# Kernel tuning notes

Measured on AMD Instinct MI355X. Metric: run time of the kernel, lower is better.

## Reference

```python
import jax, jax.numpy as jnp
import numpy as np

T, IN, OUT, M, C = 8192, 1024, 1024, 128, 32
MIN_PERIOD, MAX_PERIOD = 1.0, 1024.0
LN_EPS = 1e-5


def _linear_params(key, in_f, out_f):
    # equinox nn.Linear default init: U(-1/sqrt(in), 1/sqrt(in)) for weight and bias
    lim = 1.0 / np.sqrt(in_f)
    kw, kb = jax.random.split(key)
    w = jax.random.uniform(kw, (out_f, in_f), minval=-lim, maxval=lim, dtype=jnp.float32)
    b = jax.random.uniform(kb, (out_f,), minval=-lim, maxval=lim, dtype=jnp.float32)
    return w, b


def setup_inputs() -> dict:
    key = jax.random.key(0)
    ks = jax.random.split(key, 8)
    x = jax.random.normal(ks[0], (T, IN), dtype=jnp.float32)
    done = jax.random.bernoulli(ks[1], 0.01, (T,))  # sparse episode resets
    state_re = jnp.zeros((1, M, C), jnp.float32)
    state_im = jnp.zeros((1, M, C), jnp.float32)
    # ffa.init(memory_size, context_size): decay rates a and context frequencies b
    a = jnp.linspace(1e-6, 0.5, M, dtype=jnp.float32)
    b = 2.0 * jnp.pi / jnp.linspace(MIN_PERIOD, MAX_PERIOD, C, dtype=jnp.float32)
    pre_w, pre_b = _linear_params(ks[2], IN, M)
    gin_w, gin_b = _linear_params(ks[3], IN, M)
    gout_w, gout_b = _linear_params(ks[4], IN, OUT)
    skip_w, skip_b = _linear_params(ks[5], IN, OUT)
    mix_w, mix_b = _linear_params(ks[6], 2 * M * C, OUT)
    return dict(x=x, done=done, state_re=state_re, state_im=state_im, a=a, b=b,
                pre_w=pre_w, pre_b=pre_b, gin_w=gin_w, gin_b=gin_b,
                gout_w=gout_w, gout_b=gout_b, skip_w=skip_w, skip_b=skip_b,
                mix_w=mix_w, mix_b=mix_b)


def _ffm_forward(x, done, s0, a, b, pre_w, pre_b, gin_w, gin_b,
                 gout_w, gout_b, skip_w, skip_b, mix_w, mix_b):
    # input gating: gated_x[t, m]
    gate_in = jax.nn.sigmoid(x @ gin_w.T + gin_b)            # [T, M]
    gated_x = (x @ pre_w.T + pre_b) * gate_in                # [T, M]

    # gamma[m, c] = exp(-|a_m| + i b_c): per-step complex decay/rotation
    re, im = jnp.broadcast_arrays(-jnp.abs(a)[:, None], b[None, :])
    gamma = jnp.exp(jax.lax.complex(re, im))                 # [M, C] complex64

    def step(s, inp):
        # s_t = gamma * s_{t-1} * (1 - done_t) + x_t 1^T  (reset before accumulate)
        xt, dt = inp
        keep = jnp.where(dt, 0.0, 1.0).astype(jnp.float32)
        s = keep * s * gamma + xt[:, None]
        return s, s

    _, states = jax.lax.scan(step, s0, (gated_x.astype(jnp.complex64), done))  # [T, M, C]

    # mix: concat(real, imag) along last axis -> [T, M, 2C] -> [T, 2MC]
    z_in = jnp.concatenate([states.real, states.imag], axis=-1).reshape(states.shape[0], -1)
    z = z_in @ mix_w.T + mix_b                               # [T, OUT]

    gate_out = jax.nn.sigmoid(x @ gout_w.T + gout_b)         # [T, OUT]
    skip = x @ skip_w.T + skip_b                             # [T, OUT]

    # LayerNorm without weight/bias (eps = 1e-5)
    zg = z * gate_out
    mu = zg.mean(-1, keepdims=True)
    var = ((zg - mu) ** 2).mean(-1, keepdims=True)
    ln = (zg - mu) / jnp.sqrt(var + LN_EPS)

    out = ln + skip * (1.0 - gate_out)
    return out, states


def reference(x, done, state_re, state_im, a, b, pre_w, pre_b, gin_w, gin_b,
              gout_w, gout_b, skip_w, skip_b, mix_w, mix_b):
    s0 = jax.lax.complex(state_re, state_im)[0]              # [M, C]
    return _ffm_forward(x, done, s0, a, b, pre_w, pre_b, gin_w, gin_b,
                        gout_w, gout_b, skip_w, skip_b, mix_w, mix_b)
```

## Files before the change

### kernel.cpp

```cpp
#include <hip/hip_runtime.h>
#include <stdint.h>

#define T_DIM 8192
#define IN_DIM 1024
#define OUT_DIM 1024
#define M_DIM 128
#define SEG 64
#define NSEG (T_DIM / SEG)
#define CHUNK 2048
#define KS_FB 4

typedef __bf16 bf16x8 __attribute__((ext_vector_type(8)));
typedef float f32x4 __attribute__((ext_vector_type(4)));

__device__ inline unsigned short f2bf(float f) {
  unsigned int u = __float_as_uint(f);
  unsigned int r = (u + 0x7fffu + ((u >> 16) & 1u)) >> 16;
  return (unsigned short)r;
}
__device__ inline float bf2f(unsigned short h) {
  return __uint_as_float(((unsigned int)h) << 16);
}
__device__ inline float sigm(float v) { return 1.f / (1.f + expf(-v)); }

#define N_X   8388608L
#define N_MIX 8388608L
#define N_WGS 2359296L
__global__ __launch_bounds__(256) void prep_kernel(
    const float* __restrict__ x, const float* __restrict__ mix_w,
    const float* __restrict__ gout_w, const float* __restrict__ skip_w,
    const float* __restrict__ pre_w, const float* __restrict__ gin_w,
    const float* __restrict__ gout_b, const float* __restrict__ skip_b,
    const float* __restrict__ pre_b, const float* __restrict__ gin_b,
    const float* __restrict__ a, const float* __restrict__ b,
    unsigned short* __restrict__ x_bf, unsigned short* __restrict__ Bmix,
    unsigned short* __restrict__ Wgs, float* __restrict__ bias_gs,
    float2* __restrict__ gam, float2* __restrict__ gamL) {
  const long total = N_X + N_MIX + N_WGS + 2304 + 4096;
  for (long i = (long)blockIdx.x * 256 + threadIdx.x; i < total;
       i += (long)gridDim.x * 256) {
    if (i < N_X) {
      x_bf[i] = f2bf(x[i]);
    } else if (i < N_X + N_MIX) {
      long j = i - N_X;
      long row = j >> 13;
      int k = (int)(j & 8191);
      int src = ((k >> 6) << 6) | ((k & 1) << 5) | ((k >> 1) & 31);
      Bmix[j] = f2bf(mix_w[(row << 13) + src]);
    } else if (i < N_X + N_MIX + N_WGS) {
      long j = i - N_X - N_MIX;
      int row = (int)(j >> 10), col = (int)(j & 1023);
      float v;
      if (row < 1024)       v = gout_w[row * 1024 + col];
      else if (row < 2048)  v = skip_w[(row - 1024) * 1024 + col];
      else if (row < 2176)  v = pre_w[(row - 2048) * 1024 + col];
      else                  v = gin_w[(row - 2176) * 1024 + col];
      Wgs[j] = f2bf(v);
    } else if (i < N_X + N_MIX + N_WGS + 2304) {
      int j = (int)(i - N_X - N_MIX - N_WGS);
      float v;
      if (j < 1024)      v = gout_b[j];
      else if (j < 2048) v = skip_b[j - 1024];
      else if (j < 2176) v = pre_b[j - 2048];
      else               v = gin_b[j - 2176];
      bias_gs[j] = v;
    } else {
      int tid = (int)(i - N_X - N_MIX - N_WGS - 2304);
      int m = tid >> 5, c = tid & 31;
      double aa = fabs((double)a[m]);
      double ang = (double)b[c];
      double mag = exp(-aa);
      gam[tid] = make_float2((float)(mag * cos(ang)), (float)(mag * sin(ang)));
      double magL = exp(-aa * (double)SEG);
      double angL = ang * (double)SEG;
      gamL[tid] = make_float2((float)(magL * cos(angL)), (float)(magL * sin(angL)));
    }
  }
}

#define GEMM_KLOOP(AP, BP, LDK)                                                        \
  for (int k0 = 0; k0 < kloop_end; k0 += 64) {                                         \
    _Pragma("unroll")                                                                  \
    for (int cc = 0; cc < 4; ++cc) {                                                   \
      __builtin_amdgcn_global_load_lds(                                                \
          (const __attribute__((address_space(1))) void*)(AP + k0 + (size_t)cc * 32 * (LDK)), \
          (__attribute__((address_space(3))) void*)(As + cc * 2048 + w * 512), 16, 0, 0);     \
      __builtin_amdgcn_global_load_lds(                                                \
          (const __attribute__((address_space(1))) void*)(BP + k0 + (size_t)cc * 32 * (LDK)), \
          (__attribute__((address_space(3))) void*)(Bs + cc * 2048 + w * 512), 16, 0, 0);     \
    }                                                                                  \
    __syncthreads();                                                                   \
    _Pragma("unroll")                                                                  \
    for (int kk = 0; kk < 2; ++kk) {                                                   \
      const int eb = kk ? e1 : e0;                                                     \
      const char* Bp = (const char*)Bpbase + eb;                                       \
      bf16x8 b0 = *(const bf16x8*)(Bp);                                                \
      bf16x8 b1 = *(const bf16x8*)(Bp + 2048);                                         \
      bf16x8 b2 = *(const bf16x8*)(Bp + 4096);                                         \
      bf16x8 b3 = *(const bf16x8*)(Bp + 6144);                                         \
      const char* Ap = (const char*)Apbase + eb;                                       \
      _Pragma("unroll")                                                                \
      for (int i = 0; i < 4; ++i) {                                                    \
        bf16x8 af = *(const bf16x8*)(Ap + i * 2048);                                   \
        acc[i][0] = __builtin_amdgcn_mfma_f32_16x16x32_bf16(af, b0, acc[i][0], 0, 0, 0);\
        acc[i][1] = __builtin_amdgcn_mfma_f32_16x16x32_bf16(af, b1, acc[i][1], 0, 0, 0);\
        acc[i][2] = __builtin_amdgcn_mfma_f32_16x16x32_bf16(af, b2, acc[i][2], 0, 0, 0);\
        acc[i][3] = __builtin_amdgcn_mfma_f32_16x16x32_bf16(af, b3, acc[i][3], 0, 0, 0);\
      }                                                                                \
    }                                                                                  \
    __syncthreads();                                                                   \
  }

#define GEMM_PREAMBLE                                                                  \
  const int tid = threadIdx.x;                                                         \
  const int lane = tid & 63, w = tid >> 6;                                             \
  const int wr = w >> 1, wc = w & 1;                                                   \
  f32x4 acc[4][4] = {};                                                                \
  const int srow = tid >> 3;                                                           \
  const int ksw = ((tid & 7) ^ (srow & 7)) * 8;                                        \
  const int l15 = lane & 15;                                                           \
  const int krd = (lane >> 4) * 8;                                                     \
  const int rsw = (lane & 7) << 3;                                                     \
  const int e0 = (krd ^ rsw) * 2;                                                      \
  const int e1 = ((32 + krd) ^ rsw) * 2;                                               \
  const unsigned short* Apbase = &As[(wr * 64 + l15) * 64];                            \
  const unsigned short* Bpbase = &Bs[(wc * 64 + l15) * 64];

__global__ __launch_bounds__(256, 4) void gemm_gs_kernel(
    const unsigned short* __restrict__ A, const unsigned short* __restrict__ B,
    const float* __restrict__ bias, unsigned short* __restrict__ gs,
    float* __restrict__ tmp) {
  __shared__ __align__(16) unsigned short As[128 * 64];
  __shared__ __align__(16) unsigned short Bs[128 * 64];
  const int xcd = blockIdx.x & 7;
  const int idx = blockIdx.x >> 3;
  const int bn = idx % 18;
  const int bm = xcd * 8 + idx / 18;
  const int n0 = bn * 128, t0 = bm * 128;
  GEMM_PREAMBLE
  const unsigned short* Ab = A + (size_t)(t0 + srow) * 1024 + ksw;
  const unsigned short* Bb = B + (size_t)(n0 + srow) * 1024 + ksw;
  const int kloop_end = 1024;
  GEMM_KLOOP(Ab, Bb, 1024)

  const int rbase = t0 + wr * 64 + ((lane >> 4) * 4);
  const int cbase = n0 + wc * 64 + l15;
#pragma unroll
  for (int j = 0; j < 4; ++j) {
    const int col = cbase + j * 16;
    const float bv = bias[col];
#pragma unroll
    for (int i = 0; i < 4; ++i) {
#pragma unroll
      for (int r = 0; r < 4; ++r) {
        float v = acc[i][j][r] + bv;
        int row = rbase + i * 16 + r;
        if (col < 2048) gs[(size_t)row * 2048 + col] = f2bf(v);
        else            tmp[(size_t)row * 256 + (col - 2048)] = v;
      }
    }
  }
}

__global__ __launch_bounds__(256, 4) void gemm_splitk_kernel(
    const unsigned short* __restrict__ A, const unsigned short* __restrict__ B,
    float* __restrict__ partials, int nbm, int kslice, int prows, int xcd_map) {
  __shared__ __align__(16) unsigned short As[128 * 64];
  __shared__ __align__(16) unsigned short Bs[128 * 64];
  int bm, bn, ks;
  if (xcd_map) {
    const int xcd = blockIdx.x & 7;
    const int idx = blockIdx.x >> 3;
    ks = xcd >> 2;
    bm = (xcd & 3) * 16 + (idx >> 3);
    bn = idx & 7;
  } else {
    const int cpx = gridDim.x >> 3;
    const int wid = (blockIdx.x & 7) * cpx + (blockIdx.x >> 3);
    bm = wid % nbm;
    bn = (wid / nbm) & 7;
    ks = wid / (nbm * 8);
  }
  const int n0 = bn * 128, t0 = bm * 128;
  GEMM_PREAMBLE
  const unsigned short* Ab = A + (size_t)(t0 + srow) * 8192 + ks * kslice + ksw;
  const unsigned short* Bb = B + (size_t)(n0 + srow) * 8192 + ks * kslice + ksw;
  const int kloop_end = kslice;
  GEMM_KLOOP(Ab, Bb, 8192)

  float* Cp = partials + (size_t)ks * prows * 1024;
  const int rbase = t0 + wr * 64 + ((lane >> 4) * 4);
  const int cbase = n0 + wc * 64 + l15;
#pragma unroll
  for (int j = 0; j < 4; ++j) {
    const int col = cbase + j * 16;
#pragma unroll
    for (int i = 0; i < 4; ++i)
#pragma unroll
      for (int r = 0; r < 4; ++r)
        Cp[(size_t)(rbase + i * 16 + r) * 1024 + col] = acc[i][j][r];
  }
}

__global__ __launch_bounds__(256) void reduce_kernel(const f32x4* __restrict__ partials,
                                                     const f32x4* __restrict__ bias4,
                                                     f32x4* __restrict__ outc) {
  int i = blockIdx.x * 256 + threadIdx.x;
  const size_t stride = (size_t)CHUNK * 256;
  f32x4 s = partials[i];
#pragma unroll
  for (int p = 1; p < KS_FB; ++p) s += partials[(size_t)p * stride + i];
  s += bias4[i & 255];
  outc[i] = s;
}

__global__ __launch_bounds__(256) void gated_kernel(const float* __restrict__ tmp,
                                                    float* __restrict__ gated) {
  int i = blockIdx.x * 256 + threadIdx.x;
  int t = i >> 7, m = i & 127;
  float p = tmp[t * 256 + m];
  float g = tmp[t * 256 + 128 + m];
  gated[i] = p * sigm(g);
}

__global__ __launch_bounds__(256) void scan_p1_kernel(
    const float* __restrict__ gated, const int* __restrict__ done,
    const float2* __restrict__ gam, const float2* __restrict__ gamL,
    float2* __restrict__ carryA, float2* __restrict__ carryB) {
  int gid = blockIdx.x * 256 + threadIdx.x;
  int seg = gid >> 12, tid = gid & 4095;
  int m = tid >> 5;
  float2 g = gam[tid];
  int t0 = seg * SEG;
  float sr = 0.f, si = 0.f, keep_all = 1.f;
  for (int tt = 0; tt < SEG; ++tt) {
    int t = t0 + tt;
    float xv = gated[t * M_DIM + m];
    bool d = done[t] != 0;
    float pr = d ? 0.f : sr;
    float pi = d ? 0.f : si;
    if (d) keep_all = 0.f;
    sr = fmaf(g.x, pr, fmaf(-g.y, pi, xv));
    si = fmaf(g.y, pr, g.x * pi);
  }
  carryB[(size_t)seg * 4096 + tid] = make_float2(sr, si);
  float2 gL = gamL[tid];
  carryA[(size_t)seg * 4096 + tid] = make_float2(keep_all * gL.x, keep_all * gL.y);
}

__global__ __launch_bounds__(256) void scan_p2_kernel(
    const float2* __restrict__ carryA, float2* __restrict__ carryB,
    const float* __restrict__ s0_re, const float* __restrict__ s0_im) {
  int tid = blockIdx.x * 256 + threadIdx.x;
  float sr = s0_re[tid], si = s0_im[tid];
  float2 A0 = carryA[tid], B0 = carryB[tid];
  for (int p = 0; p < NSEG; ++p) {
    size_t nidx = (size_t)(p + 1) * 4096 + tid;
    float2 A1, B1;
    if (p + 1 < NSEG) { A1 = carryA[nidx]; B1 = carryB[nidx]; }
    carryB[(size_t)p * 4096 + tid] = make_float2(sr, si);
    float nr = fmaf(A0.x, sr, fmaf(-A0.y, si, B0.x));
    float ni = fmaf(A0.y, sr, fmaf(A0.x, si, B0.y));
    sr = nr; si = ni;
    A0 = A1; B0 = B1;
  }
}

__global__ __launch_bounds__(256) void scan_p3_kernel(
    const float* __restrict__ gated, const int* __restrict__ done,
    const float2* __restrict__ gam, const float2* __restrict__ segstart,
    float* __restrict__ out_states, int pair_mode,
    unsigned int* __restrict__ st_bf, int tbase) {
  int gid = blockIdx.x * 256 + threadIdx.x;
  int segl = gid >> 12, tid = gid & 4095;
  int m = tid >> 5;
  int seg = tbase / SEG + segl;
  float2 g = gam[tid];
  float2 s = segstart[(size_t)seg * 4096 + tid];
  float sr = s.x, si = s.y;
  int t0 = seg * SEG;
  for (int tt = 0; tt < SEG; ++tt) {
    int t = t0 + tt;
    float xv = gated[t * M_DIM + m];
    bool d = done[t] != 0;
    float pr = d ? 0.f : sr;
    float pi = d ? 0.f : si;
    sr = fmaf(g.x, pr, fmaf(-g.y, pi, xv));
    si = fmaf(g.y, pr, g.x * pi);
    if (pair_mode) {
      ((float2*)out_states)[(size_t)t * 4096 + tid] = make_float2(sr, si);
    } else {
      out_states[(size_t)t * 4096 + tid] = sr;
    }
    st_bf[(size_t)(t - tbase) * 4096 + tid] =
        (unsigned int)f2bf(sr) | ((unsigned int)f2bf(si) << 16);
  }
}

__global__ __launch_bounds__(256) void ln_kernel(const float* __restrict__ partials, int nred,
                                                 const float* __restrict__ mixb,
                                                 const unsigned short* __restrict__ gs,
                                                 float* __restrict__ out) {
  const int t = blockIdx.x;
  const int tid = threadIdx.x;
  __shared__ float sm[8];
  const int o = tid * 4;
  f32x4 z;
  if (nred == 0) {
    z = *(const f32x4*)&out[(size_t)t * 1024 + o];
  } else {
    z = *(const f32x4*)&partials[(size_t)t * 1024 + o];
    for (int p = 1; p < nred; ++p)
      z += *(const f32x4*)&partials[(size_t)p * T_DIM * 1024 + (size_t)t * 1024 + o];
    z += *(const f32x4*)&mixb[o];
  }
  ushort4 gu = *(const ushort4*)&gs[(size_t)t * 2048 + o];
  ushort4 su = *(const ushort4*)&gs[(size_t)t * 2048 + 1024 + o];
  float g[4], sk[4], zg[4];
  g[0] = sigm(bf2f(gu.x)); g[1] = sigm(bf2f(gu.y));
  g[2] = sigm(bf2f(gu.z)); g[3] = sigm(bf2f(gu.w));
  sk[0] = bf2f(su.x); sk[1] = bf2f(su.y); sk[2] = bf2f(su.z); sk[3] = bf2f(su.w);
  float sum = 0.f;
#pragma unroll
  for (int j = 0; j < 4; ++j) { zg[j] = z[j] * g[j]; sum += zg[j]; }
#pragma unroll
  for (int off = 32; off > 0; off >>= 1) sum += __shfl_down(sum, off, 64);
  if ((tid & 63) == 0) sm[tid >> 6] = sum;
  __syncthreads();
  const float mu = (sm[0] + sm[1] + sm[2] + sm[3]) * (1.f / 1024.f);
  float sq = 0.f;
#pragma unroll
  for (int j = 0; j < 4; ++j) { float d = zg[j] - mu; sq += d * d; }
#pragma unroll
  for (int off = 32; off > 0; off >>= 1) sq += __shfl_down(sq, off, 64);
  if ((tid & 63) == 0) sm[4 + (tid >> 6)] = sq;
  __syncthreads();
  const float var = (sm[4] + sm[5] + sm[6] + sm[7]) * (1.f / 1024.f);
  const float rstd = 1.f / sqrtf(var + 1e-5f);
  f32x4 res;
#pragma unroll
  for (int j = 0; j < 4; ++j) res[j] = (zg[j] - mu) * rstd + sk[j] * (1.f - g[j]);
  *(f32x4*)&out[(size_t)t * 1024 + o] = res;
}

extern "C" void kernel_launch(void* const* d_in, const int* in_sizes, int n_in,
                              void* d_out, int out_size, void* d_ws, size_t ws_size,
                              hipStream_t stream) {
  const float* x      = (const float*)d_in[0];
  const int*   done   = (const int*)d_in[1];
  const float* s0_re  = (const float*)d_in[2];
  const float* s0_im  = (const float*)d_in[3];
  const float* a      = (const float*)d_in[4];
  const float* b      = (const float*)d_in[5];
  const float* pre_w  = (const float*)d_in[6];
  const float* pre_b  = (const float*)d_in[7];
  const float* gin_w  = (const float*)d_in[8];
  const float* gin_b  = (const float*)d_in[9];
  const float* gout_w = (const float*)d_in[10];
  const float* gout_b = (const float*)d_in[11];
  const float* skip_w = (const float*)d_in[12];
  const float* skip_b = (const float*)d_in[13];
  const float* mix_w  = (const float*)d_in[14];
  const float* mix_b  = (const float*)d_in[15];

  float* out_f = (float*)d_out;
  float* states_f = out_f + (size_t)T_DIM * OUT_DIM;
  const int pair_mode = (out_size >= 75000000) ? 1 : 0;

  char* ws = (char*)d_ws;
  size_t off = 0;
  auto alloc = [&](size_t bytes) {
    void* p = ws + off;
    off = (off + bytes + 255) & ~(size_t)255;
    return p;
  };
  unsigned short* x_bf   = (unsigned short*)alloc((size_t)T_DIM * IN_DIM * 2);
  unsigned short* Bmix   = (unsigned short*)alloc((size_t)OUT_DIM * 8192 * 2);
  unsigned short* Wgs    = (unsigned short*)alloc((size_t)2304 * IN_DIM * 2);
  float* bias_gs         = (float*)alloc(2304 * 4);
  float* tmp_pg          = (float*)alloc((size_t)T_DIM * 256 * 4);
  float* gated           = (float*)alloc((size_t)T_DIM * M_DIM * 4);
  float2* gam            = (float2*)alloc(4096 * 8);
  float2* gamL           = (float2*)alloc(4096 * 8);
  float2* carryA         = (float2*)alloc((size_t)NSEG * 4096 * 8);
  float2* carryB         = (float2*)alloc((size_t)NSEG * 4096 * 8);
  unsigned short* gs_o   = (unsigned short*)alloc((size_t)T_DIM * 2048 * 2);

  size_t need_main = off + (size_t)T_DIM * 8192 * 2 + (size_t)2 * T_DIM * 1024 * 4 + 1024;
  const int full_path = (ws_size == 0 || ws_size >= need_main) ? 1 : 0;

  dim3 blk(256);
  prep_kernel<<<2048, blk, 0, stream>>>(x, mix_w, gout_w, skip_w, pre_w, gin_w,
                                        gout_b, skip_b, pre_b, gin_b, a, b,
                                        x_bf, Bmix, Wgs, bias_gs, gam, gamL);

  gemm_gs_kernel<<<1152, blk, 0, stream>>>(x_bf, Wgs, bias_gs, gs_o, tmp_pg);
  gated_kernel<<<(T_DIM * M_DIM) / 256, blk, 0, stream>>>(tmp_pg, gated);

  scan_p1_kernel<<<NSEG * 16, blk, 0, stream>>>(gated, done, gam, gamL, carryA, carryB);
  scan_p2_kernel<<<16, blk, 0, stream>>>(carryA, carryB, s0_re, s0_im);

  if (full_path) {
    unsigned short* st_bf = (unsigned short*)alloc((size_t)T_DIM * 8192 * 2);
    float* partials       = (float*)alloc((size_t)2 * T_DIM * 1024 * 4);
    scan_p3_kernel<<<NSEG * 16, blk, 0, stream>>>(gated, done, gam, carryB,
                                                  states_f, pair_mode,
                                                  (unsigned int*)st_bf, 0);
    gemm_splitk_kernel<<<1024, blk, 0, stream>>>(st_bf, Bmix, partials,
                                                 64, 4096, T_DIM, 1);
    ln_kernel<<<T_DIM, blk, 0, stream>>>(partials, 2, mix_b, gs_o, out_f);
  } else {
    unsigned short* st_bf = (unsigned short*)alloc((size_t)CHUNK * 8192 * 2);
    float* partials       = (float*)alloc((size_t)KS_FB * CHUNK * 1024 * 4);
    for (int ch = 0; ch < T_DIM / CHUNK; ++ch) {
      int tbase = ch * CHUNK;
      scan_p3_kernel<<<(CHUNK / SEG) * 16, blk, 0, stream>>>(gated, done, gam, carryB,
                                                             states_f, pair_mode,
                                                             (unsigned int*)st_bf, tbase);
      gemm_splitk_kernel<<<8 * (CHUNK / 128) * KS_FB, blk, 0, stream>>>(
          st_bf, Bmix, partials, CHUNK / 128, 8192 / KS_FB, CHUNK, 0);
      reduce_kernel<<<CHUNK, blk, 0, stream>>>((const f32x4*)partials, (const f32x4*)mix_b,
                                               (f32x4*)(out_f + (size_t)tbase * OUT_DIM));
    }
    ln_kernel<<<T_DIM, blk, 0, stream>>>(nullptr, 0, mix_b, gs_o, out_f);
  }
  (void)n_in; (void)in_sizes;
}
```

Before: 374.5 us.

## Replace mix split-K GEMM with 256x256-tile pipelined kernel using LDS prefetch

```diff
diff --git a/kernel.cpp b/kernel.cpp
--- a/kernel.cpp
+++ b/kernel.cpp
@@ -162,25 +162,170 @@
   }
 }
 
+__global__ __launch_bounds__(512, 1) void gemm_mix256_kernel(
+    const unsigned short* __restrict__ A, const unsigned short* __restrict__ B,
+    float* __restrict__ partials) {
+  __shared__ __align__(16) unsigned short As[3][256 * 64];
+  __shared__ __align__(16) unsigned short Bs[2][256 * 64];
+  const int xcd = blockIdx.x & 7;
+  const int idx = blockIdx.x >> 3;
+  const int ks = xcd >> 2;
+  const int bm = (xcd & 3) * 8 + (idx >> 2);
+  const int bn = idx & 3;
+  const int t0 = bm * 256, n0 = bn * 256;
+  const int tid = threadIdx.x;
+  const int lane = tid & 63;
+  const int w8 = tid >> 6;
+  const int wr = w8 >> 2;
+  const int wcol = w8 & 3;
+
+  f32x4 acc[8][4] = {};
+
+  const int srow = tid >> 3;
+  const int ksw = ((tid & 7) ^ (srow & 7)) * 8;
+  const unsigned short* Ab = A + (size_t)(t0 + srow) * 8192 + ks * 4096 + ksw;
+  const unsigned short* Bb = B + (size_t)(n0 + srow) * 8192 + ks * 4096 + ksw;
+
+  const int l15 = lane & 15;
+  const int krd = (lane >> 4) * 8;
+  const int rsw = (lane & 7) << 3;
+  const int e0 = (krd ^ rsw) * 2;
+  const int e1 = ((32 + krd) ^ rsw) * 2;
+
+#define ISS_A(buf, kt, j)                                                               \
+  __builtin_amdgcn_global_load_lds(                                                    \
+      (const __attribute__((address_space(1))) void*)(Ab + (kt) + (size_t)(j) * 64 * 8192), \
+      (__attribute__((address_space(3))) void*)(&As[buf][(j) * 4096 + tid * 8]), 16, 0, 0);
+#define ISS_B(buf, kt, j)                                                               \
+  __builtin_amdgcn_global_load_lds(                                                    \
+      (const __attribute__((address_space(1))) void*)(Bb + (kt) + (size_t)(j) * 64 * 8192), \
+      (__attribute__((address_space(3))) void*)(&Bs[buf][(j) * 4096 + tid * 8]), 16, 0, 0);
+
+#define MFMA16(IB)                                                                      \
+  acc[IB+0][0] = __builtin_amdgcn_mfma_f32_16x16x32_bf16(af0, bf0, acc[IB+0][0], 0,0,0); \
+  acc[IB+0][1] = __builtin_amdgcn_mfma_f32_16x16x32_bf16(af0, bf1, acc[IB+0][1], 0,0,0); \
+  acc[IB+0][2] = __builtin_amdgcn_mfma_f32_16x16x32_bf16(af0, bf2, acc[IB+0][2], 0,0,0); \
+  acc[IB+0][3] = __builtin_amdgcn_mfma_f32_16x16x32_bf16(af0, bf3, acc[IB+0][3], 0,0,0); \
+  acc[IB+1][0] = __builtin_amdgcn_mfma_f32_16x16x32_bf16(af1, bf0, acc[IB+1][0], 0,0,0); \
+  acc[IB+1][1] = __builtin_amdgcn_mfma_f32_16x16x32_bf16(af1, bf1, acc[IB+1][1], 0,0,0); \
+  acc[IB+1][2] = __builtin_amdgcn_mfma_f32_16x16x32_bf16(af1, bf2, acc[IB+1][2], 0,0,0); \
+  acc[IB+1][3] = __builtin_amdgcn_mfma_f32_16x16x32_bf16(af1, bf3, acc[IB+1][3], 0,0,0); \
+  acc[IB+2][0] = __builtin_amdgcn_mfma_f32_16x16x32_bf16(af2, bf0, acc[IB+2][0], 0,0,0); \
+  acc[IB+2][1] = __builtin_amdgcn_mfma_f32_16x16x32_bf16(af2, bf1, acc[IB+2][1], 0,0,0); \
+  acc[IB+2][2] = __builtin_amdgcn_mfma_f32_16x16x32_bf16(af2, bf2, acc[IB+2][2], 0,0,0); \
+  acc[IB+2][3] = __builtin_amdgcn_mfma_f32_16x16x32_bf16(af2, bf3, acc[IB+2][3], 0,0,0); \
+  acc[IB+3][0] = __builtin_amdgcn_mfma_f32_16x16x32_bf16(af3, bf0, acc[IB+3][0], 0,0,0); \
+  acc[IB+3][1] = __builtin_amdgcn_mfma_f32_16x16x32_bf16(af3, bf1, acc[IB+3][1], 0,0,0); \
+  acc[IB+3][2] = __builtin_amdgcn_mfma_f32_16x16x32_bf16(af3, bf2, acc[IB+3][2], 0,0,0); \
+  acc[IB+3][3] = __builtin_amdgcn_mfma_f32_16x16x32_bf16(af3, bf3, acc[IB+3][3], 0,0,0);
+
+#define PHASE_TAIL                                                                      \
+  __builtin_amdgcn_s_barrier();                                                         \
+  asm volatile("s_waitcnt lgkmcnt(0)" ::: "memory");                                    \
+  __builtin_amdgcn_sched_barrier(0);                                                    \
+  __builtin_amdgcn_s_setprio(1);
+#define PHASE_END                                                                       \
+  __builtin_amdgcn_s_setprio(0);                                                        \
+  __builtin_amdgcn_s_barrier();
+
+  const int iters = 64;
+  ISS_A(0, 0, 0) ISS_A(0, 0, 1) ISS_A(0, 0, 2) ISS_A(0, 0, 3)
+  ISS_B(0, 0, 0) ISS_B(0, 0, 1) ISS_B(0, 0, 2) ISS_B(0, 0, 3)
+  ISS_A(1, 64, 0) ISS_A(1, 64, 1) ISS_A(1, 64, 2) ISS_A(1, 64, 3)
+
+  int abuf = 0;
+  for (int t = 0; t < iters; ++t) {
+    const int bbuf = t & 1;
+    asm volatile("s_waitcnt vmcnt(4)" ::: "memory");
+    __builtin_amdgcn_s_barrier();
+    __builtin_amdgcn_sched_barrier(0);
+
+    const char* Apb = (const char*)&As[abuf][(wr * 128 + l15) * 64];
+    const char* Bpb = (const char*)&Bs[bbuf][(wcol * 64 + l15) * 64];
+    const int tb = (t + 1 < iters) ? (t + 1) * 64 : t * 64;
+    const int ta = (t + 2 < iters) ? (t + 2) * 64 : t * 64;
+    const int nb = (t + 1) & 1;
+    int na = abuf + 2; if (na >= 3) na -= 3;
+
+    bf16x8 bf0, bf1, bf2, bf3, af0, af1, af2, af3;
+
+    bf0 = *(const bf16x8*)(Bpb + e0);
+    bf1 = *(const bf16x8*)(Bpb + 2048 + e0);
+    bf2 = *(const bf16x8*)(Bpb + 4096 + e0);
+    bf3 = *(const bf16x8*)(Bpb + 6144 + e0);
+    af0 = *(const bf16x8*)(Apb + e0);
+    af1 = *(const bf16x8*)(Apb + 2048 + e0);
+    af2 = *(const bf16x8*)(Apb + 4096 + e0);
+    af3 = *(const bf16x8*)(Apb + 6144 + e0);
+    ISS_B(nb, tb, 0) ISS_B(nb, tb, 1)
+    PHASE_TAIL
+    MFMA16(0)
+    PHASE_END
+
+    af0 = *(const bf16x8*)(Apb + 8192 + e0);
+    af1 = *(const bf16x8*)(Apb + 10240 + e0);
+    af2 = *(const bf16x8*)(Apb + 12288 + e0);
+    af3 = *(const bf16x8*)(Apb + 14336 + e0);
+    ISS_B(nb, tb, 2) ISS_B(nb, tb, 3)
+    PHASE_TAIL
+    MFMA16(4)
+    PHASE_END
+
+    bf0 = *(const bf16x8*)(Bpb + e1);
+    bf1 = *(const bf16x8*)(Bpb + 2048 + e1);
+    bf2 = *(const bf16x8*)(Bpb + 4096 + e1);
+    bf3 = *(const bf16x8*)(Bpb + 6144 + e1);
+    af0 = *(const bf16x8*)(Apb + e1);
+    af1 = *(const bf16x8*)(Apb + 2048 + e1);
+    af2 = *(const bf16x8*)(Apb + 4096 + e1);
+    af3 = *(const bf16x8*)(Apb + 6144 + e1);
+    ISS_A(na, ta, 0) ISS_A(na, ta, 1)
+    PHASE_TAIL
+    MFMA16(0)
+    PHASE_END
+
+    af0 = *(const bf16x8*)(Apb + 8192 + e1);
+    af1 = *(const bf16x8*)(Apb + 10240 + e1);
+    af2 = *(const bf16x8*)(Apb + 12288 + e1);
+    af3 = *(const bf16x8*)(Apb + 14336 + e1);
+    ISS_A(na, ta, 2) ISS_A(na, ta, 3)
+    PHASE_TAIL
+    MFMA16(4)
+    PHASE_END
+
+    abuf += 1; if (abuf >= 3) abuf -= 3;
+  }
+  asm volatile("s_waitcnt vmcnt(0)" ::: "memory");
+
+  float* Cp = partials + (size_t)ks * T_DIM * 1024;
+  const int rbase = t0 + wr * 128 + ((lane >> 4) * 4);
+  const int cbase = n0 + wcol * 64 + l15;
+#pragma unroll
+  for (int j = 0; j < 4; ++j) {
+    const int col = cbase + j * 16;
+#pragma unroll
+    for (int i = 0; i < 8; ++i)
+#pragma unroll
+      for (int r = 0; r < 4; ++r)
+        Cp[(size_t)(rbase + i * 16 + r) * 1024 + col] = acc[i][j][r];
+  }
+#undef ISS_A
+#undef ISS_B
+#undef MFMA16
+#undef PHASE_TAIL
+#undef PHASE_END
+}
+
 __global__ __launch_bounds__(256, 4) void gemm_splitk_kernel(
     const unsigned short* __restrict__ A, const unsigned short* __restrict__ B,
-    float* __restrict__ partials, int nbm, int kslice, int prows, int xcd_map) {
+    float* __restrict__ partials, int nbm, int kslice, int prows) {
   __shared__ __align__(16) unsigned short As[128 * 64];
   __shared__ __align__(16) unsigned short Bs[128 * 64];
-  int bm, bn, ks;
-  if (xcd_map) {
-    const int xcd = blockIdx.x & 7;
-    const int idx = blockIdx.x >> 3;
-    ks = xcd >> 2;
-    bm = (xcd & 3) * 16 + (idx >> 3);
-    bn = idx & 7;
-  } else {
-    const int cpx = gridDim.x >> 3;
-    const int wid = (blockIdx.x & 7) * cpx + (blockIdx.x >> 3);
-    bm = wid % nbm;
-    bn = (wid / nbm) & 7;
-    ks = wid / (nbm * 8);
-  }
+  const int cpx = gridDim.x >> 3;
+  const int wid = (blockIdx.x & 7) * cpx + (blockIdx.x >> 3);
+  const int bm = wid % nbm;
+  const int bn = (wid / nbm) & 7;
+  const int ks = wid / (nbm * 8);
   const int n0 = bn * 128, t0 = bm * 128;
   GEMM_PREAMBLE
   const unsigned short* Ab = A + (size_t)(t0 + srow) * 8192 + ks * kslice + ksw;
@@ -406,8 +551,7 @@
     scan_p3_kernel<<<NSEG * 16, blk, 0, stream>>>(gated, done, gam, carryB,
                                                   states_f, pair_mode,
                                                   (unsigned int*)st_bf, 0);
-    gemm_splitk_kernel<<<1024, blk, 0, stream>>>(st_bf, Bmix, partials,
-                                                 64, 4096, T_DIM, 1);
+    gemm_mix256_kernel<<<256, dim3(512), 0, stream>>>(st_bf, Bmix, partials);
     ln_kernel<<<T_DIM, blk, 0, stream>>>(partials, 2, mix_b, gs_o, out_f);
   } else {
     unsigned short* st_bf = (unsigned short*)alloc((size_t)CHUNK * 8192 * 2);
@@ -418,7 +562,7 @@
                                                              states_f, pair_mode,
                                                              (unsigned int*)st_bf, tbase);
       gemm_splitk_kernel<<<8 * (CHUNK / 128) * KS_FB, blk, 0, stream>>>(
-          st_bf, Bmix, partials, CHUNK / 128, 8192 / KS_FB, CHUNK, 0);
+          st_bf, Bmix, partials, CHUNK / 128, 8192 / KS_FB, CHUNK);
       reduce_kernel<<<CHUNK, blk, 0, stream>>>((const f32x4*)partials, (const f32x4*)mix_b,
                                                (f32x4*)(out_f + (size_t)tbase * OUT_DIM));
     }
```

Result: faster. 364.0 us, median of 2 (-2.8%).
